# Optimization experiments

Measured on AMD Instinct MI355X. Metric: run time of the kernel, lower is better.

The kernel has to match this reference:

```python
import jax, jax.numpy as jnp
import numpy as np

BITS = 8
QMAX = float(2 ** (BITS - 1) - 1)  # 127 for 8-bit symmetric


def bits_quant(x):
    """8-bit symmetric per-tensor fake quantization (models the opaque bits_quant op)."""
    max_abs = jnp.max(jnp.abs(x))
    scale = jnp.where(max_abs > 0, max_abs / QMAX, 1.0).astype(x.dtype)
    q = jnp.clip(jnp.round(x / scale), -QMAX, QMAX) * scale
    return q


def quant_linear(x, w, b):
    # Q(Q(x @ w) + Q(b)) then Q of the result, per QuantLinearLayer.call
    y = bits_quant(jnp.matmul(x, w)) + bits_quant(b)
    return bits_quant(y)


def setup_inputs() -> dict:
    d = 4096
    key = jax.random.key(0)
    ks = jax.random.split(key, 12)
    s = 0.02
    return {
        "inputs": jax.random.normal(ks[0], (1, d), dtype=jnp.float32),
        "c": jax.random.normal(ks[1], (1, d), dtype=jnp.float32) * s,
        "h": jax.random.normal(ks[2], (1, d), dtype=jnp.float32) * s,
        "Wf_w": jax.random.normal(ks[3], (2 * d, d), dtype=jnp.float32) * s,
        "Wf_b": jax.random.normal(ks[4], (d,), dtype=jnp.float32) * s,
        "Wi_w": jax.random.normal(ks[5], (2 * d, d), dtype=jnp.float32) * s,
        "Wi_b": jax.random.normal(ks[6], (d,), dtype=jnp.float32) * s,
        "Wc_w": jax.random.normal(ks[7], (2 * d, d), dtype=jnp.float32) * s,
        "Wc_b": jax.random.normal(ks[8], (d,), dtype=jnp.float32) * s,
        "Wo_w": jax.random.normal(ks[9], (2 * d, d), dtype=jnp.float32) * s,
        "Wo_b": jax.random.normal(ks[10], (d,), dtype=jnp.float32) * s,
    }


def reference(inputs, c, h, Wf_w, Wf_b, Wi_w, Wi_b, Wc_w, Wc_b, Wo_w, Wo_b):
    # concat = Q([h, x])  -> [1, 2d]
    concat = bits_quant(jnp.concatenate([h, inputs], axis=1))
    z = bits_quant(jnp.tanh(quant_linear(concat, Wc_w, Wc_b)))
    zf = bits_quant(jax.nn.sigmoid(quant_linear(concat, Wf_w, Wf_b)))
    zi = bits_quant(jax.nn.sigmoid(quant_linear(concat, Wi_w, Wi_b)))
    zo = bits_quant(jax.nn.sigmoid(quant_linear(concat, Wo_w, Wo_b)))
    memory = bits_quant(z * zi)
    c_new = bits_quant(bits_quant(c * zf) + memory)
    h_new = bits_quant(zo * bits_quant(jnp.tanh(c_new)))
    return h_new
```

## Files before the change

### kernel.cpp

```cpp
#include <hip/hip_runtime.h>
#include <math.h>

#define QMAXF 127.0f

struct Ptrs4 { const float* p[4]; };

__device__ __forceinline__ float qscale(float m) {
    return (m > 0.0f) ? (m / QMAXF) : 1.0f;
}

__device__ __forceinline__ float quant1(float x, float s) {
    float r = rintf(x / s);
    r = fminf(fmaxf(r, -QMAXF), QMAXF);
    return r * s;
}

__device__ __forceinline__ float block_max_red(float v, float* sred) {
    #pragma unroll
    for (int off = 32; off > 0; off >>= 1)
        v = fmaxf(v, __shfl_down(v, off, 64));
    int wave = threadIdx.x >> 6;
    int lane = threadIdx.x & 63;
    __syncthreads();
    if (lane == 0) sred[wave] = v;
    __syncthreads();
    if (threadIdx.x == 0) {
        int nw = blockDim.x >> 6;
        float m = sred[0];
        for (int i = 1; i < nw; ++i) m = fmaxf(m, sred[i]);
        sred[16] = m;
    }
    __syncthreads();
    return sred[16];
}

__device__ __forceinline__ void quant_vec4(float* a, float* sred) {
    float pm = 0.0f;
    #pragma unroll
    for (int i = 0; i < 4; ++i) pm = fmaxf(pm, fabsf(a[i]));
    float s = qscale(block_max_red(pm, sred));
    #pragma unroll
    for (int i = 0; i < 4; ++i) a[i] = quant1(a[i], s);
}

__global__ __launch_bounds__(1024) void k_prep(
    const float* __restrict__ x, const float* __restrict__ h,
    Ptrs4 biases, float* __restrict__ concat_q, float* __restrict__ qb,
    unsigned* __restrict__ gmax)
{
    __shared__ float sred[17];
    int tid = threadIdx.x;
    if (blockIdx.x == 0) {
        if (tid < 4) gmax[tid] = 0u;
        float vals[8];
        float pm = 0.0f;
        #pragma unroll
        for (int i = 0; i < 8; ++i) {
            int idx = i * 1024 + tid;
            float v = (i < 4) ? h[idx] : x[idx - 4096];
            vals[i] = v;
            pm = fmaxf(pm, fabsf(v));
        }
        float s = qscale(block_max_red(pm, sred));
        #pragma unroll
        for (int i = 0; i < 8; ++i) concat_q[i * 1024 + tid] = quant1(vals[i], s);
    } else {
        int g = blockIdx.x - 1;
        const float* __restrict__ b = biases.p[g];
        float vals[4];
        float pm = 0.0f;
        #pragma unroll
        for (int i = 0; i < 4; ++i) {
            float v = b[i * 1024 + tid];
            vals[i] = v;
            pm = fmaxf(pm, fabsf(v));
        }
        float s = qscale(block_max_red(pm, sred));
        #pragma unroll
        for (int i = 0; i < 4; ++i) qb[g * 4096 + i * 1024 + tid] = quant1(vals[i], s);
    }
}

#define KCHUNKS 64
#define KB      (8192 / KCHUNKS)

__global__ __launch_bounds__(256) void k_gemv(
    Ptrs4 wts, const float* __restrict__ xq, float* __restrict__ partials)
{
    int ct = blockIdx.x;
    int kc = blockIdx.y;
    int g  = blockIdx.z;
    const float* __restrict__ W = wts.p[g];
    int col0 = ct * 1024 + threadIdx.x * 4;
    int k0 = kc * KB;
    const float* __restrict__ wrow = W + (size_t)k0 * 4096 + col0;
    const float* __restrict__ xp = xq + k0;

    float ax = 0.f, ay = 0.f, az = 0.f, aw = 0.f;
    float4 cur[4], nxt[4];

    #pragma unroll
    for (int j = 0; j < 4; ++j)
        cur[j] = *(const float4*)(wrow + (size_t)j * 4096);

    for (int kk = 0; kk < KB - 4; kk += 4) {
        #pragma unroll
        for (int j = 0; j < 4; ++j)
            nxt[j] = *(const float4*)(wrow + (size_t)(kk + 4 + j) * 4096);
        #pragma unroll
        for (int j = 0; j < 4; ++j) {
            float xv = xp[kk + j];
            ax = fmaf(xv, cur[j].x, ax);
            ay = fmaf(xv, cur[j].y, ay);
            az = fmaf(xv, cur[j].z, az);
            aw = fmaf(xv, cur[j].w, aw);
        }
        #pragma unroll
        for (int j = 0; j < 4; ++j) cur[j] = nxt[j];
    }
    #pragma unroll
    for (int j = 0; j < 4; ++j) {
        float xv = xp[KB - 4 + j];
        ax = fmaf(xv, cur[j].x, ax);
        ay = fmaf(xv, cur[j].y, ay);
        az = fmaf(xv, cur[j].z, az);
        aw = fmaf(xv, cur[j].w, aw);
    }

    float4 r; r.x = ax; r.y = ay; r.z = az; r.w = aw;
    *(float4*)(partials + (size_t)(g * KCHUNKS + kc) * 4096 + col0) = r;
}

__global__ __launch_bounds__(256) void k_reduce(
    const float* __restrict__ partials, float* __restrict__ y,
    unsigned* __restrict__ gmax)
{
    int g  = blockIdx.x >> 4;
    int cb = blockIdx.x & 15;
    int col = cb * 256 + threadIdx.x;
    float s = 0.0f;
    #pragma unroll 8
    for (int kc = 0; kc < KCHUNKS; ++kc)
        s += partials[(size_t)(g * KCHUNKS + kc) * 4096 + col];
    y[g * 4096 + col] = s;

    float m = fabsf(s);
    #pragma unroll
    for (int off = 32; off > 0; off >>= 1)
        m = fmaxf(m, __shfl_down(m, off, 64));
    __shared__ float sm[4];
    int wave = threadIdx.x >> 6, lane = threadIdx.x & 63;
    if (lane == 0) sm[wave] = m;
    __syncthreads();
    if (threadIdx.x == 0) {
        float mm = fmaxf(fmaxf(sm[0], sm[1]), fmaxf(sm[2], sm[3]));
        atomicMax(gmax + g, __float_as_uint(mm));
    }
}

__global__ __launch_bounds__(1024) void k_epilogue(
    const float* __restrict__ y, const float* __restrict__ qb,
    const unsigned* __restrict__ gmax, const float* __restrict__ c,
    float* __restrict__ out)
{
    __shared__ float sred[17];
    int tid = threadIdx.x;
    float v[4][4];

    #pragma unroll
    for (int g = 0; g < 4; ++g) {
        float s = qscale(__uint_as_float(gmax[g]));
        #pragma unroll
        for (int i = 0; i < 4; ++i) {
            int col = i * 1024 + tid;
            v[g][i] = quant1(y[g * 4096 + col], s) + qb[g * 4096 + col];
        }
    }

    for (int g = 0; g < 4; ++g) {
        float pm = 0.0f;
        #pragma unroll
        for (int i = 0; i < 4; ++i) pm = fmaxf(pm, fabsf(v[g][i]));
        float s = qscale(block_max_red(pm, sred));
        #pragma unroll
        for (int i = 0; i < 4; ++i) {
            float q = quant1(v[g][i], s);
            v[g][i] = (g == 2) ? tanhf(q) : (1.0f / (1.0f + expf(-q)));
        }
    }

    for (int g = 0; g < 4; ++g) {
        float pm = 0.0f;
        #pragma unroll
        for (int i = 0; i < 4; ++i) pm = fmaxf(pm, fabsf(v[g][i]));
        float s = qscale(block_max_red(pm, sred));
        #pragma unroll
        for (int i = 0; i < 4; ++i) v[g][i] = quant1(v[g][i], s);
    }

    float mem[4];
    #pragma unroll
    for (int i = 0; i < 4; ++i) mem[i] = v[2][i] * v[1][i];
    quant_vec4(mem, sred);

    float cf[4];
    #pragma unroll
    for (int i = 0; i < 4; ++i) cf[i] = c[i * 1024 + tid] * v[0][i];
    quant_vec4(cf, sred);

    float cn[4];
    #pragma unroll
    for (int i = 0; i < 4; ++i) cn[i] = cf[i] + mem[i];
    quant_vec4(cn, sred);

    float tc[4];
    #pragma unroll
    for (int i = 0; i < 4; ++i) tc[i] = tanhf(cn[i]);
    quant_vec4(tc, sred);

    float hn[4];
    #pragma unroll
    for (int i = 0; i < 4; ++i) hn[i] = v[3][i] * tc[i];
    quant_vec4(hn, sred);
    #pragma unroll
    for (int i = 0; i < 4; ++i) out[i * 1024 + tid] = hn[i];
}

extern "C" void kernel_launch(void* const* d_in, const int* in_sizes, int n_in,
                              void* d_out, int out_size, void* d_ws, size_t ws_size,
                              hipStream_t stream) {
    const float* x = (const float*)d_in[0];
    const float* c = (const float*)d_in[1];
    const float* h = (const float*)d_in[2];
    Ptrs4 wts, bs;
    wts.p[0] = (const float*)d_in[3];  bs.p[0] = (const float*)d_in[4];
    wts.p[1] = (const float*)d_in[5];  bs.p[1] = (const float*)d_in[6];
    wts.p[2] = (const float*)d_in[7];  bs.p[2] = (const float*)d_in[8];
    wts.p[3] = (const float*)d_in[9];  bs.p[3] = (const float*)d_in[10];

    float* ws = (float*)d_ws;
    float* partials = ws;
    float* concat_q = ws + 1048576;
    float* qb       = ws + 1048576 + 8192;
    float* yv       = ws + 1048576 + 8192 + 16384;
    unsigned* gmax  = (unsigned*)(ws + 1048576 + 8192 + 16384 + 16384);

    hipLaunchKernelGGL(k_prep,     dim3(5),              dim3(1024), 0, stream,
                       x, h, bs, concat_q, qb, gmax);
    hipLaunchKernelGGL(k_gemv,     dim3(4, KCHUNKS, 4),  dim3(256),  0, stream,
                       wts, concat_q, partials);
    hipLaunchKernelGGL(k_reduce,   dim3(64),             dim3(256),  0, stream,
                       partials, yv, gmax);
    hipLaunchKernelGGL(k_epilogue, dim3(1),              dim3(1024), 0, stream,
                       yv, qb, gmax, c, (float*)d_out);
}
```

Measured before the change: 494.2 us.

## Restructure GEMV so each block covers all columns with per-wave row interleave

Each GEMV block now handles a whole 128-row K chunk across all 4096 columns. Each wave takes every fourth row and reads full contiguous 4 KB rows with 16 float4 loads per lane, double-buffered in registers. The four wave partials are then combined through a 64 KB shared-memory array before one partials row is written. The grid drops from 1024 to 256 blocks with launch_bounds(256,1), so there is fewer but wider in-flight memory traffic per block, at the cost of much higher register use and less occupancy for hiding the weight stream.

```diff
diff --git a/kernel.cpp b/kernel.cpp
--- a/kernel.cpp
+++ b/kernel.cpp
@@ -82,53 +82,102 @@
 }
 
 #define KCHUNKS 64
-#define KB      (8192 / KCHUNKS)
-
-__global__ __launch_bounds__(256) void k_gemv(
+#define RPB (8192 / KCHUNKS)
+#define RPW (RPB / 4)
+
+__global__ __launch_bounds__(256, 1) void k_gemv(
     Ptrs4 wts, const float* __restrict__ xq, float* __restrict__ partials)
 {
-    int ct = blockIdx.x;
-    int kc = blockIdx.y;
-    int g  = blockIdx.z;
+    int kc = blockIdx.x;
+    int g  = blockIdx.y;
     const float* __restrict__ W = wts.p[g];
-    int col0 = ct * 1024 + threadIdx.x * 4;
-    int k0 = kc * KB;
-    const float* __restrict__ wrow = W + (size_t)k0 * 4096 + col0;
-    const float* __restrict__ xp = xq + k0;
-
-    float ax = 0.f, ay = 0.f, az = 0.f, aw = 0.f;
-    float4 cur[4], nxt[4];
-
-    #pragma unroll
-    for (int j = 0; j < 4; ++j)
-        cur[j] = *(const float4*)(wrow + (size_t)j * 4096);
-
-    for (int kk = 0; kk < KB - 4; kk += 4) {
-        #pragma unroll
-        for (int j = 0; j < 4; ++j)
-            nxt[j] = *(const float4*)(wrow + (size_t)(kk + 4 + j) * 4096);
-        #pragma unroll
-        for (int j = 0; j < 4; ++j) {
-            float xv = xp[kk + j];
-            ax = fmaf(xv, cur[j].x, ax);
-            ay = fmaf(xv, cur[j].y, ay);
-            az = fmaf(xv, cur[j].z, az);
-            aw = fmaf(xv, cur[j].w, aw);
-        }
-        #pragma unroll
-        for (int j = 0; j < 4; ++j) cur[j] = nxt[j];
-    }
-    #pragma unroll
-    for (int j = 0; j < 4; ++j) {
-        float xv = xp[KB - 4 + j];
-        ax = fmaf(xv, cur[j].x, ax);
-        ay = fmaf(xv, cur[j].y, ay);
-        az = fmaf(xv, cur[j].z, az);
-        aw = fmaf(xv, cur[j].w, aw);
-    }
-
-    float4 r; r.x = ax; r.y = ay; r.z = az; r.w = aw;
-    *(float4*)(partials + (size_t)(g * KCHUNKS + kc) * 4096 + col0) = r;
+    int wave = threadIdx.x >> 6;
+    int lane = threadIdx.x & 63;
+
+    const float* __restrict__ rbase =
+        W + (size_t)(kc * RPB + wave) * 4096 + lane * 4;
+    const float* __restrict__ xp = xq + kc * RPB + wave;
+
+    float4 acc[16];
+    #pragma unroll
+    for (int i = 0; i < 16; ++i) acc[i] = make_float4(0.f, 0.f, 0.f, 0.f);
+
+    float4 bufA[16], bufB[16];
+    #pragma unroll
+    for (int i = 0; i < 16; ++i)
+        bufA[i] = *(const float4*)(rbase + i * 256);
+
+    for (int r = 0; r < RPW - 2; r += 2) {
+        const float* b1 = rbase + (size_t)(r + 1) * 4 * 4096;
+        #pragma unroll
+        for (int i = 0; i < 16; ++i)
+            bufB[i] = *(const float4*)(b1 + i * 256);
+        float xv0 = xp[4 * r];
+        #pragma unroll
+        for (int i = 0; i < 16; ++i) {
+            acc[i].x = fmaf(xv0, bufA[i].x, acc[i].x);
+            acc[i].y = fmaf(xv0, bufA[i].y, acc[i].y);
+            acc[i].z = fmaf(xv0, bufA[i].z, acc[i].z);
+            acc[i].w = fmaf(xv0, bufA[i].w, acc[i].w);
+        }
+        const float* b2 = rbase + (size_t)(r + 2) * 4 * 4096;
+        #pragma unroll
+        for (int i = 0; i < 16; ++i)
+            bufA[i] = *(const float4*)(b2 + i * 256);
+        float xv1 = xp[4 * (r + 1)];
+        #pragma unroll
+        for (int i = 0; i < 16; ++i) {
+            acc[i].x = fmaf(xv1, bufB[i].x, acc[i].x);
+            acc[i].y = fmaf(xv1, bufB[i].y, acc[i].y);
+            acc[i].z = fmaf(xv1, bufB[i].z, acc[i].z);
+            acc[i].w = fmaf(xv1, bufB[i].w, acc[i].w);
+        }
+    }
+    {
+        const float* b1 = rbase + (size_t)(RPW - 1) * 4 * 4096;
+        #pragma unroll
+        for (int i = 0; i < 16; ++i)
+            bufB[i] = *(const float4*)(b1 + i * 256);
+        float xv0 = xp[4 * (RPW - 2)];
+        #pragma unroll
+        for (int i = 0; i < 16; ++i) {
+            acc[i].x = fmaf(xv0, bufA[i].x, acc[i].x);
+            acc[i].y = fmaf(xv0, bufA[i].y, acc[i].y);
+            acc[i].z = fmaf(xv0, bufA[i].z, acc[i].z);
+            acc[i].w = fmaf(xv0, bufA[i].w, acc[i].w);
+        }
+        float xv1 = xp[4 * (RPW - 1)];
+        #pragma unroll
+        for (int i = 0; i < 16; ++i) {
+            acc[i].x = fmaf(xv1, bufB[i].x, acc[i].x);
+            acc[i].y = fmaf(xv1, bufB[i].y, acc[i].y);
+            acc[i].z = fmaf(xv1, bufB[i].z, acc[i].z);
+            acc[i].w = fmaf(xv1, bufB[i].w, acc[i].w);
+        }
+    }
+
+    __shared__ float red[4][4096];
+    #pragma unroll
+    for (int i = 0; i < 16; ++i)
+        *(float4*)&red[wave][i * 256 + lane * 4] = acc[i];
+    __syncthreads();
+
+    float* __restrict__ pout = partials + (size_t)(g * KCHUNKS + kc) * 4096;
+    int t = threadIdx.x;
+    #pragma unroll
+    for (int q = 0; q < 4; ++q) {
+        int col = q * 1024 + t * 4;
+        float4 s0 = *(const float4*)&red[0][col];
+        float4 s1 = *(const float4*)&red[1][col];
+        float4 s2 = *(const float4*)&red[2][col];
+        float4 s3 = *(const float4*)&red[3][col];
+        float4 r4;
+        r4.x = (s0.x + s1.x) + (s2.x + s3.x);
+        r4.y = (s0.y + s1.y) + (s2.y + s3.y);
+        r4.z = (s0.z + s1.z) + (s2.z + s3.z);
+        r4.w = (s0.w + s1.w) + (s2.w + s3.w);
+        *(float4*)(pout + col) = r4;
+    }
 }
 
 __global__ __launch_bounds__(256) void k_reduce(
@@ -245,12 +294,12 @@
     float* yv       = ws + 1048576 + 8192 + 16384;
     unsigned* gmax  = (unsigned*)(ws + 1048576 + 8192 + 16384 + 16384);
 
-    hipLaunchKernelGGL(k_prep,     dim3(5),              dim3(1024), 0, stream,
+    hipLaunchKernelGGL(k_prep,     dim3(5),           dim3(1024), 0, stream,
                        x, h, bs, concat_q, qb, gmax);
-    hipLaunchKernelGGL(k_gemv,     dim3(4, KCHUNKS, 4),  dim3(256),  0, stream,
+    hipLaunchKernelGGL(k_gemv,     dim3(KCHUNKS, 4),  dim3(256),  0, stream,
                        wts, concat_q, partials);
-    hipLaunchKernelGGL(k_reduce,   dim3(64),             dim3(256),  0, stream,
+    hipLaunchKernelGGL(k_reduce,   dim3(64),          dim3(256),  0, stream,
                        partials, yv, gmax);
-    hipLaunchKernelGGL(k_epilogue, dim3(1),              dim3(1024), 0, stream,
+    hipLaunchKernelGGL(k_epilogue, dim3(1),           dim3(1024), 0, stream,
                        yv, qb, gmax, c, (float*)d_out);
 }
```

Measured after the change: 472.4 us. 4.4% less time.
